# Kernel optimization log

Measured on AMD Instinct MI355X. Metric: run time of the kernel, lower is better.

## Reference

```python
import jax, jax.numpy as jnp
import numpy as np

N_BATCH = 1024   # batch size (P=256 identities x K=4 instances)
M_PARTS = 8      # local stripes per image
D_FEAT = 128     # local feature dim
K_PER_ID = 4
MARGIN = 0.3
EPS = 1e-12


def setup_inputs() -> dict:
    key = jax.random.key(0)
    inputs = jax.random.normal(key, (N_BATCH, M_PARTS, D_FEAT), dtype=jnp.float32)
    labels = jnp.arange(N_BATCH, dtype=jnp.int64) // K_PER_ID  # equal samples per class
    return {"inputs": inputs, "labels": labels}


def _shortest_dist(dmat):
    """DTW-style monotone shortest path over the (m, n) grid.
    dmat: [m, n, N, N] -> returns [N, N].
    """
    m = dmat.shape[0]
    # first row: only moves to the right -> cumulative sum over j
    row = jnp.cumsum(dmat[0], axis=0)  # [n, N, N]
    inf = jnp.full(dmat.shape[2:], jnp.inf, dtype=dmat.dtype)

    def step(carry, inp):
        d_ij, up = inp                       # each [N, N]
        val = jnp.minimum(carry, up) + d_ij  # carry=inf at j=0 -> picks `up`
        return val, val

    for i in range(1, m):  # m is a small structural constant (stripes)
        _, row = jax.lax.scan(step, inf, (dmat[i], row))
    return row[-1]  # dist[m-1][n-1], shape [N, N]


def _local_dist(x):
    """x: [N, m, d] (already L2-normalized) -> pairwise aligned dist [N, N]."""
    N, m, d = x.shape
    xf = x.reshape(N * m, d)
    sq = jnp.sum(xf * xf, axis=1)
    dist = sq[:, None] + sq[None, :] - 2.0 * (xf @ xf.T)   # [Nm, Nm]
    dist = jnp.sqrt(jnp.clip(dist, EPS, None))
    dist = jnp.tanh(dist * 0.5)  # (e^d - 1) / (e^d + 1)
    dist = dist.reshape(N, m, N, m).transpose(1, 3, 0, 2)   # [m, n, N, N]
    return _shortest_dist(dist)


def reference(inputs, labels):
    # normalize local features to unit length
    x = inputs / (jnp.linalg.norm(inputs, axis=-1, keepdims=True) + EPS)
    dist_mat = _local_dist(x)  # [N, N]

    # hard example mining
    is_pos = labels[:, None] == labels[None, :]
    dist_ap = jnp.max(jnp.where(is_pos, dist_mat, -jnp.inf), axis=1)
    dist_an = jnp.min(jnp.where(is_pos, jnp.inf, dist_mat), axis=1)

    # MarginRankingLoss(margin)(dist_an, dist_ap, y=1)
    loss = jnp.mean(jnp.maximum(dist_ap - dist_an + MARGIN, 0.0))
    return loss
```

## Files before the change

kernel.cpp:

```cpp
#include <hip/hip_runtime.h>
#include <hip/hip_bf16.h>
#include <math.h>

#define NB 1024
#define MP 8
#define DF 128
#define NV (NB*MP)
#define EPSR 1e-12f
#define MARGIN_ 0.3f

#define GC0  0.4999965f
#define GC1 -0.0416276f
#define GC2  0.0040808f
#define GC3 -0.00035138f
#define GC4  0.00001765f

typedef __bf16 bf16x8 __attribute__((ext_vector_type(8)));
typedef float  f32x4  __attribute__((ext_vector_type(4)));

__global__ __launch_bounds__(256) void norm_kernel(const float* __restrict__ x,
                                                   unsigned short* __restrict__ xnb,
                                                   float* __restrict__ sq,
                                                   float* __restrict__ out) {
    if (blockIdx.x == 0 && threadIdx.x == 0) out[0] = 0.0f;
    const int wave = threadIdx.x >> 6;
    const int lane = threadIdx.x & 63;
    const int v = blockIdx.x * 4 + wave;
    const float e0 = x[v * DF + lane];
    const float e1 = x[v * DF + 64 + lane];
    float s = e0 * e0 + e1 * e1;
    #pragma unroll
    for (int off = 32; off > 0; off >>= 1) s += __shfl_xor(s, off);
    const float inv = 1.0f / (sqrtf(s) + EPSR);
    const __hip_bfloat16 b0 = __float2bfloat16(e0 * inv);
    const __hip_bfloat16 b1 = __float2bfloat16(e1 * inv);
    xnb[v * DF + lane]      = *(const unsigned short*)&b0;
    xnb[v * DF + 64 + lane] = *(const unsigned short*)&b1;
    if (lane == 0) sq[v] = s * inv * inv;
}

__global__ __launch_bounds__(256) void dist_kernel(const unsigned short* __restrict__ xnb,
                                                   const float* __restrict__ sq,
                                                   float* __restrict__ dist) {
    __shared__ alignas(16) unsigned char smem[65536];
    unsigned short* As = (unsigned short*)smem;
    unsigned short* Bs = (unsigned short*)(smem + 32768);
    float* E = (float*)smem;

    const int idx = (int)blockIdx.x;
    float fsq = sqrtf(8.0f * (float)idx + 1.0f);
    int by = (int)((fsq - 1.0f) * 0.5f);
    while ((by + 1) * (by + 2) / 2 <= idx) ++by;
    while (by * (by + 1) / 2 > idx) --by;
    const int bx = idx - by * (by + 1) / 2;

    const int t    = threadIdx.x;
    const int wave = t >> 6;
    const int lane = t & 63;
    const int wr   = wave >> 1;
    const int wc   = wave & 1;
    const int aBase = bx * 16;
    const int bBase = by * 16;

    #pragma unroll
    for (int i = 0; i < 8; ++i) {
        const int ldi = t + i * 256;
        const int row = ldi >> 4;
        const int ch  = ldi & 15;
        const int p   = ch ^ (row & 15);
        const uint4 va = *(const uint4*)&xnb[(aBase * MP + row) * DF + ch * 8];
        const uint4 vb = *(const uint4*)&xnb[(bBase * MP + row) * DF + ch * 8];
        *(uint4*)&As[row * DF + p * 8] = va;
        *(uint4*)&Bs[row * DF + p * 8] = vb;
    }
    __syncthreads();

    f32x4 acc[4][4];
    #pragma unroll
    for (int tr = 0; tr < 4; ++tr)
        #pragma unroll
        for (int tc = 0; tc < 4; ++tc) acc[tr][tc] = (f32x4){0.f, 0.f, 0.f, 0.f};

    const int fr = lane & 15;
    const int fq = lane >> 4;
    #pragma unroll
    for (int ks = 0; ks < 4; ++ks) {
        bf16x8 af[4], bfr[4];
        const int ch = ks * 4 + fq;
        #pragma unroll
        for (int tr = 0; tr < 4; ++tr) {
            const int va = wr * 64 + tr * 16 + fr;
            af[tr] = *(const bf16x8*)&As[va * DF + (ch ^ fr) * 8];
        }
        #pragma unroll
        for (int tc = 0; tc < 4; ++tc) {
            const int vb = wc * 64 + tc * 16 + fr;
            bfr[tc] = *(const bf16x8*)&Bs[vb * DF + (ch ^ fr) * 8];
        }
        #pragma unroll
        for (int tr = 0; tr < 4; ++tr)
            #pragma unroll
            for (int tc = 0; tc < 4; ++tc)
                acc[tr][tc] = __builtin_amdgcn_mfma_f32_16x16x32_bf16(
                    af[tr], bfr[tc], acc[tr][tc], 0, 0, 0);
    }
    __syncthreads();

    #pragma unroll
    for (int tr = 0; tr < 4; ++tr) {
        const int r0 = wr * 64 + tr * 16 + fq * 4;
        const int aL = r0 >> 3;
        const int cqr = fq & 1;
        #pragma unroll
        for (int tc = 0; tc < 4; ++tc) {
            const int c  = wc * 64 + tc * 16 + fr;
            const int bL = c >> 3, j = c & 7;
            const int cq = (j << 1) | cqr;
            const int p  = (cq ^ bL) & 15;
            *(f32x4*)&E[(((aL << 4) + bL) << 6) + (p << 2)] = acc[tr][tc];
        }
    }
    __syncthreads();

    const int aG = aBase + (t >> 4);
    const int bG = bBase + (t & 15);
    float sa[8], sb[8];
    #pragma unroll
    for (int i = 0; i < 8; ++i) {
        sa[i] = sq[aG * MP + i];
        sb[i] = sq[bG * MP + i];
    }

    float g8[8][8];
    {
        const int bL = t & 15;
        #pragma unroll
        for (int cq = 0; cq < 16; ++cq) {
            const int p = (cq ^ bL) & 15;
            const f32x4 v = *(const f32x4*)&E[(t << 6) + (p << 2)];
            const int j = cq >> 1, ib = (cq & 1) * 4;
            #pragma unroll
            for (int g = 0; g < 4; ++g) {
                const int i = ib + g;
                const float d2 = fmaxf(fmaf(-2.0f, v[g], sa[i] + sb[j]), EPSR);
                const float d  = __builtin_amdgcn_sqrtf(d2);
                const float pg = fmaf(fmaf(fmaf(fmaf(GC4, d2, GC3), d2, GC2),
                                           d2, GC1), d2, GC0);
                g8[i][j] = d * pg;
            }
        }
    }

    float rowv[8];
    {
        float c = 0.0f;
        #pragma unroll
        for (int j = 0; j < 8; ++j) { c += g8[0][j]; rowv[j] = c; }
    }
    #pragma unroll
    for (int i = 1; i < 8; ++i) {
        float carry = INFINITY;
        #pragma unroll
        for (int j = 0; j < 8; ++j) {
            const float v = fminf(carry, rowv[j]) + g8[i][j];
            rowv[j] = v;
            carry = v;
        }
    }
    dist[aG * NB + bG] = rowv[7];
    if (bx != by) dist[bG * NB + aG] = rowv[7];
}

__global__ __launch_bounds__(256) void mine_kernel(const float* __restrict__ dist,
                                                   const int* __restrict__ labels,
                                                   float* __restrict__ out) {
    __shared__ float buf[4];
    const int wave = threadIdx.x >> 6;
    const int lane = threadIdx.x & 63;
    const int a = blockIdx.x * 4 + wave;
    const int la = labels[a];
    float mx = -INFINITY;
    float mn =  INFINITY;
    #pragma unroll
    for (int bb = 0; bb < NB / 64; ++bb) {
        const int b = bb * 64 + lane;
        const float d = dist[a * NB + b];
        if (labels[b] == la) mx = fmaxf(mx, d);
        else                 mn = fminf(mn, d);
    }
    #pragma unroll
    for (int off = 32; off > 0; off >>= 1) {
        mx = fmaxf(mx, __shfl_xor(mx, off));
        mn = fminf(mn, __shfl_xor(mn, off));
    }
    if (lane == 0) buf[wave] = fmaxf(mx - mn + MARGIN_, 0.0f);
    __syncthreads();
    if (threadIdx.x == 0) {
        atomicAdd(out, (buf[0] + buf[1] + buf[2] + buf[3]) * (1.0f / (float)NB));
    }
}

extern "C" void kernel_launch(void* const* d_in, const int* in_sizes, int n_in,
                              void* d_out, int out_size, void* d_ws, size_t ws_size,
                              hipStream_t stream) {
    const float* x      = (const float*)d_in[0];
    const int*   labels = (const int*)d_in[1];
    float* out = (float*)d_out;

    unsigned short* xnb = (unsigned short*)d_ws;
    float* sq   = (float*)(xnb + (size_t)NV * DF);
    float* dist = sq + NV;

    const int ntiles = (NB / 16) * (NB / 16 + 1) / 2;

    norm_kernel<<<NV / 4, 256, 0, stream>>>(x, xnb, sq, out);
    dist_kernel<<<ntiles, 256, 0, stream>>>(xnb, sq, dist);
    mine_kernel<<<NB / 4, 256, 0, stream>>>(dist, labels, out);
}
```

Before: 87.88 us.

## Fuse hard-example mining into distance kernel via atomic min/max reductions

The hard positive/negative mining is folded into the distance kernel. Each tile reduces its per-row max-positive and min-negative with shuffles, then updates global per-anchor arrays with integer atomicMin/atomicMax on float bit patterns, valid because the distances are non-negative. This removes the 4MB NxN distance matrix write and re-read, and a single-block kernel computes the final loss. The squared norms are also replaced by the constant 1 (d2 = 2 - 2·dot), on the assumption that the normalized vectors are unit length. That adds a small error from bf16 rounding and the eps term, and it brings in atomic contention.

```diff
diff --git a/kernel.cpp b/kernel.cpp
--- a/kernel.cpp
+++ b/kernel.cpp
@@ -20,9 +20,14 @@
 
 __global__ __launch_bounds__(256) void norm_kernel(const float* __restrict__ x,
                                                    unsigned short* __restrict__ xnb,
-                                                   float* __restrict__ sq,
-                                                   float* __restrict__ out) {
-    if (blockIdx.x == 0 && threadIdx.x == 0) out[0] = 0.0f;
+                                                   unsigned* __restrict__ ap_max,
+                                                   unsigned* __restrict__ an_min) {
+    if (blockIdx.x == 0) {
+        for (int i = threadIdx.x; i < NB; i += 256) {
+            ap_max[i] = 0u;
+            an_min[i] = 0x7F800000u;
+        }
+    }
     const int wave = threadIdx.x >> 6;
     const int lane = threadIdx.x & 63;
     const int v = blockIdx.x * 4 + wave;
@@ -36,12 +41,12 @@
     const __hip_bfloat16 b1 = __float2bfloat16(e1 * inv);
     xnb[v * DF + lane]      = *(const unsigned short*)&b0;
     xnb[v * DF + 64 + lane] = *(const unsigned short*)&b1;
-    if (lane == 0) sq[v] = s * inv * inv;
 }
 
 __global__ __launch_bounds__(256) void dist_kernel(const unsigned short* __restrict__ xnb,
-                                                   const float* __restrict__ sq,
-                                                   float* __restrict__ dist) {
+                                                   const int* __restrict__ labels,
+                                                   unsigned* __restrict__ ap_max,
+                                                   unsigned* __restrict__ an_min) {
     __shared__ alignas(16) unsigned char smem[65536];
     unsigned short* As = (unsigned short*)smem;
     unsigned short* Bs = (unsigned short*)(smem + 32768);
@@ -122,15 +127,6 @@
     }
     __syncthreads();
 
-    const int aG = aBase + (t >> 4);
-    const int bG = bBase + (t & 15);
-    float sa[8], sb[8];
-    #pragma unroll
-    for (int i = 0; i < 8; ++i) {
-        sa[i] = sq[aG * MP + i];
-        sb[i] = sq[bG * MP + i];
-    }
-
     float g8[8][8];
     {
         const int bL = t & 15;
@@ -141,12 +137,11 @@
             const int j = cq >> 1, ib = (cq & 1) * 4;
             #pragma unroll
             for (int g = 0; g < 4; ++g) {
-                const int i = ib + g;
-                const float d2 = fmaxf(fmaf(-2.0f, v[g], sa[i] + sb[j]), EPSR);
+                const float d2 = fmaxf(fmaf(-2.0f, v[g], 2.0f), EPSR);
                 const float d  = __builtin_amdgcn_sqrtf(d2);
                 const float pg = fmaf(fmaf(fmaf(fmaf(GC4, d2, GC3), d2, GC2),
                                            d2, GC1), d2, GC0);
-                g8[i][j] = d * pg;
+                g8[ib + g][j] = d * pg;
             }
         }
     }
@@ -167,36 +162,57 @@
             carry = v;
         }
     }
-    dist[aG * NB + bG] = rowv[7];
-    if (bx != by) dist[bG * NB + aG] = rowv[7];
-}
-
-__global__ __launch_bounds__(256) void mine_kernel(const float* __restrict__ dist,
-                                                   const int* __restrict__ labels,
+    const float d = rowv[7];
+
+    const int aG = aBase + (t >> 4);
+    const int bG = bBase + (t & 15);
+    const bool pos = (labels[aG] == labels[bG]);
+
+    float an_v = pos ? INFINITY : d;
+    float ap_v = pos ? d : 0.0f;
+    #pragma unroll
+    for (int off = 1; off <= 8; off <<= 1) {
+        an_v = fminf(an_v, __shfl_xor(an_v, off));
+        ap_v = fmaxf(ap_v, __shfl_xor(ap_v, off));
+    }
+    if ((t & 15) == 0) {
+        atomicMin(&an_min[aG], __float_as_uint(an_v));
+        if (ap_v > 0.0f) atomicMax(&ap_max[aG], __float_as_uint(ap_v));
+    }
+
+    if (bx != by) {
+        float an_m = pos ? INFINITY : d;
+        float ap_m = pos ? d : 0.0f;
+        an_m = fminf(an_m, __shfl_xor(an_m, 16));
+        an_m = fminf(an_m, __shfl_xor(an_m, 32));
+        ap_m = fmaxf(ap_m, __shfl_xor(ap_m, 16));
+        ap_m = fmaxf(ap_m, __shfl_xor(ap_m, 32));
+        if (lane < 16) {
+            const int bG2 = bBase + lane;
+            atomicMin(&an_min[bG2], __float_as_uint(an_m));
+            if (ap_m > 0.0f) atomicMax(&ap_max[bG2], __float_as_uint(ap_m));
+        }
+    }
+}
+
+__global__ __launch_bounds__(256) void loss_kernel(const unsigned* __restrict__ ap_max,
+                                                   const unsigned* __restrict__ an_min,
                                                    float* __restrict__ out) {
     __shared__ float buf[4];
     const int wave = threadIdx.x >> 6;
     const int lane = threadIdx.x & 63;
-    const int a = blockIdx.x * 4 + wave;
-    const int la = labels[a];
-    float mx = -INFINITY;
-    float mn =  INFINITY;
-    #pragma unroll
-    for (int bb = 0; bb < NB / 64; ++bb) {
-        const int b = bb * 64 + lane;
-        const float d = dist[a * NB + b];
-        if (labels[b] == la) mx = fmaxf(mx, d);
-        else                 mn = fminf(mn, d);
-    }
-    #pragma unroll
-    for (int off = 32; off > 0; off >>= 1) {
-        mx = fmaxf(mx, __shfl_xor(mx, off));
-        mn = fminf(mn, __shfl_xor(mn, off));
-    }
-    if (lane == 0) buf[wave] = fmaxf(mx - mn + MARGIN_, 0.0f);
+    float s = 0.0f;
+    for (int i = threadIdx.x; i < NB; i += 256) {
+        const float ap = __uint_as_float(ap_max[i]);
+        const float an = __uint_as_float(an_min[i]);
+        s += fmaxf(ap - an + MARGIN_, 0.0f);
+    }
+    #pragma unroll
+    for (int off = 32; off > 0; off >>= 1) s += __shfl_xor(s, off);
+    if (lane == 0) buf[wave] = s;
     __syncthreads();
     if (threadIdx.x == 0) {
-        atomicAdd(out, (buf[0] + buf[1] + buf[2] + buf[3]) * (1.0f / (float)NB));
+        out[0] = (buf[0] + buf[1] + buf[2] + buf[3]) * (1.0f / (float)NB);
     }
 }
 
@@ -208,12 +224,12 @@
     float* out = (float*)d_out;
 
     unsigned short* xnb = (unsigned short*)d_ws;
-    float* sq   = (float*)(xnb + (size_t)NV * DF);
-    float* dist = sq + NV;
+    unsigned* ap_max = (unsigned*)(xnb + (size_t)NV * DF);
+    unsigned* an_min = ap_max + NB;
 
     const int ntiles = (NB / 16) * (NB / 16 + 1) / 2;
 
-    norm_kernel<<<NV / 4, 256, 0, stream>>>(x, xnb, sq, out);
-    dist_kernel<<<ntiles, 256, 0, stream>>>(xnb, sq, dist);
-    mine_kernel<<<NB / 4, 256, 0, stream>>>(dist, labels, out);
-}
+    norm_kernel<<<NV / 4, 256, 0, stream>>>(x, xnb, ap_max, an_min);
+    dist_kernel<<<ntiles, 256, 0, stream>>>(xnb, labels, ap_max, an_min);
+    loss_kernel<<<1, 256, 0, stream>>>(ap_max, an_min, out);
+}
```

Result: no change. 88.54 us (+0.7%).
